# Kernel tuning notes

Hardware: AMD Instinct MI355X
Metric: run time of the kernel (lower is better)

## Reference

```python
import jax, jax.numpy as jnp
import numpy as np

TAU = 1.0
TOP_K = 2

def setup_inputs() -> dict:
    key = jax.random.key(0)
    ks = jax.random.split(key, 5)
    B, C, H, W, E, GH = 16, 64, 128, 128, 8, 16
    return {
        "x": jax.random.normal(ks[0], (B, C, H, W), dtype=jnp.float32),
        "wg1": jax.random.normal(ks[1], (C, GH), dtype=jnp.float32) * 0.1,
        "bg1": jnp.zeros((GH,), dtype=jnp.float32),
        "wg2": jax.random.normal(ks[2], (GH, E), dtype=jnp.float32) * 0.1,
        "bg2": jnp.zeros((E,), dtype=jnp.float32),
        "w_exp": jax.random.normal(ks[3], (E, C, C, 3, 3), dtype=jnp.float32) * 0.05,
        "b_exp": jnp.zeros((E, C), dtype=jnp.float32),
    }

def reference(x, wg1, bg1, wg2, bg2, w_exp, b_exp):
    B, C, H, W = x.shape
    E = w_exp.shape[0]
    # in_proj / out_proj are Identity (c1 == mid_channels == c2)
    x_proj = x
    # gate: GAP -> Linear -> ReLU -> Linear
    pooled = x_proj.mean(axis=(2, 3))                      # [B, C]
    h = jax.nn.relu(pooled @ wg1 + bg1)                    # [B, GH]
    gate_logits = h @ wg2 + bg2                            # [B, E]
    # soft top-k routing (hard=False)
    gate_probs = jax.nn.softmax(gate_logits / TAU, axis=-1)
    _, topk_idx = jax.lax.top_k(gate_probs, TOP_K)         # [B, K]
    mask = jnp.zeros_like(gate_probs).at[jnp.arange(B)[:, None], topk_idx].set(1.0)
    sparse_probs = gate_probs * mask
    sparse_probs = sparse_probs / (sparse_probs.sum(axis=-1, keepdims=True) + 1e-8)
    # dense all-expert 3x3 conv: fold experts into one grouped-output conv
    kern = w_exp.reshape(E * C, C, 3, 3)                   # [E*C, C, 3, 3]
    y = jax.lax.conv_general_dilated(
        x_proj, kern, window_strides=(1, 1), padding="SAME",
        dimension_numbers=("NCHW", "OIHW", "NCHW"))
    y = y.reshape(B, E, C, H, W) + b_exp[None, :, :, None, None]
    # vectorized weighted combine (replaces the per-sample python loop)
    out = jnp.einsum("be,bechw->bchw", sparse_probs, y)
    # shortcut (c1 == c2)
    return out + x
```

## Files before the change

kernel.cpp:

```cpp
#include <hip/hip_runtime.h>
#include <hip/hip_bf16.h>
#include <math.h>

#define B_  16
#define C_  64
#define HW_ 128
#define E_  8
#define GH_ 16

typedef __attribute__((ext_vector_type(8))) short short8;
typedef __attribute__((ext_vector_type(4))) float float4v;

#define ROWS_LDS 4
#define COLS_LDS 132
#define XS_SHORTS (ROWS_LDS * COLS_LDS * 32)
#define WB_PER_B (9 * 2 * 4 * 64 * 8)

__global__ __launch_bounds__(256) void pool_kernel(const float* __restrict__ x,
                                                   float* __restrict__ pooled) {
  const int bc = blockIdx.x;
  const float4v* p4 = (const float4v*)(x + (size_t)bc * (HW_ * HW_));
  float4v s4 = {0.f, 0.f, 0.f, 0.f};
  for (int i = threadIdx.x; i < (HW_ * HW_) / 4; i += 256) s4 += p4[i];
  float s = (s4.x + s4.y) + (s4.z + s4.w);
#pragma unroll
  for (int off = 32; off > 0; off >>= 1) s += __shfl_down(s, off, 64);
  __shared__ float red[4];
  if ((threadIdx.x & 63) == 0) red[threadIdx.x >> 6] = s;
  __syncthreads();
  if (threadIdx.x == 0)
    pooled[bc] = (red[0] + red[1] + red[2] + red[3]) * (1.0f / (HW_ * HW_));
}

__global__ __launch_bounds__(256) void combine_kernel(
    const float* __restrict__ w_exp, const float* __restrict__ pooled,
    const float* __restrict__ wg1, const float* __restrict__ bg1,
    const float* __restrict__ wg2, const float* __restrict__ bg2,
    const float* __restrict__ b_exp, __hip_bfloat16* __restrict__ wB,
    float* __restrict__ bcomb) {
  __shared__ float wtmp[8 * 576];
  __shared__ float hsh[GH_];
  __shared__ float psh[E_];
  const int t = threadIdx.x;
  const int b = blockIdx.x >> 3;
  const int cog = blockIdx.x & 7;

  if (t < GH_) {
    float s = bg1[t];
    for (int c = 0; c < C_; c++)
      s = fmaf(pooled[b * C_ + c], wg1[c * GH_ + t], s);
    hsh[t] = fmaxf(s, 0.f);
  }
  __syncthreads();
  if (t == 0) {
    float p[E_];
    float mx = -1e30f;
#pragma unroll
    for (int e = 0; e < E_; e++) {
      float s = bg2[e];
#pragma unroll
      for (int g = 0; g < GH_; g++) s = fmaf(hsh[g], wg2[g * E_ + e], s);
      p[e] = s;
      mx = fmaxf(mx, s);
    }
    float sum = 0.f;
#pragma unroll
    for (int e = 0; e < E_; e++) { p[e] = expf(p[e] - mx); sum += p[e]; }
    const float inv = 1.0f / sum;
#pragma unroll
    for (int e = 0; e < E_; e++) p[e] *= inv;
    int i1 = 0;
#pragma unroll
    for (int e = 1; e < E_; e++) if (p[e] > p[i1]) i1 = e;
    int i2 = -1;
#pragma unroll
    for (int e = 0; e < E_; e++) {
      if (e == i1) continue;
      if (i2 < 0 || p[e] > p[i2]) i2 = e;
    }
    const float denom = p[i1] + p[i2] + 1e-8f;
#pragma unroll
    for (int e = 0; e < E_; e++)
      psh[e] = (e == i1 || e == i2) ? (p[e] / denom) : 0.f;
  }
  __syncthreads();
  float pb[E_];
#pragma unroll
  for (int e = 0; e < E_; e++) pb[e] = psh[e];

  const size_t src0 = (size_t)cog * 8 * 576;
  for (int i = t; i < 4608; i += 256) {
    float s = 0.f;
#pragma unroll
    for (int e = 0; e < E_; e++)
      s = fmaf(pb[e], w_exp[(size_t)e * (C_ * 576) + src0 + i], s);
    wtmp[i] = s;
  }
  __syncthreads();
  for (int i = t; i < 4608; i += 256) {
    const int j = i & 7;
    const int co_l = (i >> 3) & 7;
    const int rest = i >> 6;
    const int quad = rest & 3;
    const int khalf = (rest >> 2) & 1;
    const int pos = rest >> 3;
    const int ci = khalf * 32 + quad * 8 + j;
    const int co = cog * 8 + co_l;
    float v = wtmp[co_l * 576 + ci * 9 + pos];
    if (pos == 4 && co == ci) v += 1.0f;
    wB[(size_t)b * WB_PER_B +
       ((((pos * 2 + khalf) * 4 + quad) * 64) + co) * 8 + j] =
        __float2bfloat16(v);
  }
  if (t < 8) {
    const int co = cog * 8 + t;
    float s = 0.f;
#pragma unroll
    for (int e = 0; e < E_; e++) s = fmaf(pb[e], b_exp[e * C_ + co], s);
    bcomb[b * C_ + co] = s;
  }
}

__global__ __launch_bounds__(256, 4) void conv_kernel(
    const float* __restrict__ x, const __hip_bfloat16* __restrict__ wB,
    const float* __restrict__ bcomb, float* __restrict__ out) {
  __shared__ __align__(16) short xs[XS_SHORTS];

  const int t = threadIdx.x;
  const int blk = blockIdx.x;
  const int xcd = blk & 7;
  const int idx = blk >> 3;
  const int b = xcd * 2 + (idx >> 6);
  const int strip = idx & 63;
  const int ty = strip * 2;

  const int wave = t >> 6;
  const int L = t & 63;
  const int n16 = L & 15;
  const int quad = L >> 4;

  float bias[4];
#pragma unroll
  for (int nt = 0; nt < 4; nt++) bias[nt] = bcomb[b * C_ + nt * 16 + n16];

  float4v acc[4][4];
#pragma unroll
  for (int mt = 0; mt < 4; mt++)
#pragma unroll
    for (int nt = 0; nt < 4; nt++) acc[mt][nt] = (float4v)0.f;

  for (int h = 0; h < 2; h++) {
    __syncthreads();
#pragma unroll
    for (int it = 0; it < 2; it++) {
      const int i = it * 256 + t;
      const int scq = i & 31;
      const int grp = (i >> 5) & 3;
      const int r = i >> 7;
      const int gh = ty + r - 1;
      const int ci = h * 32 + grp * 8;
      float4v v[8];
      if ((unsigned)gh < (unsigned)HW_) {
        const float* p =
            x + ((size_t)(b * C_ + ci) * HW_ + gh) * HW_ + scq * 4;
#pragma unroll
        for (int k = 0; k < 8; k++)
          v[k] = *(const float4v*)(p + (size_t)k * (HW_ * HW_));
      } else {
#pragma unroll
        for (int k = 0; k < 8; k++) v[k] = (float4v)0.f;
      }
      const int slot = grp ^ (scq & 3);
#pragma unroll
      for (int kk = 0; kk < 4; kk++) {
        const int cl = scq * 4 + kk + 1;
        short8 pk;
#pragma unroll
        for (int k = 0; k < 8; k++) {
          __hip_bfloat16 bb = __float2bfloat16(v[k][kk]);
          pk[k] = *(short*)&bb;
        }
        *(short8*)&xs[((r * COLS_LDS + cl) * 4 + slot) * 8] = pk;
      }
    }
    if (t < 32) {
      const int r = t >> 3;
      const int edge = (t >> 2) & 1;
      const int slot = t & 3;
      const int cl = edge ? 129 : 0;
      *(short8*)&xs[((r * COLS_LDS + cl) * 4 + slot) * 8] = (short8)0;
    }
    __syncthreads();

    const __hip_bfloat16* wBh =
        wB + (size_t)b * WB_PER_B + (size_t)(h * 4 + quad) * 512 + n16 * 8;
    short8 bf[2][4];
#pragma unroll
    for (int nt = 0; nt < 4; nt++)
      bf[0][nt] = *(const short8*)(wBh + nt * 128);

#pragma unroll
    for (int pos = 0; pos < 9; pos++) {
      const int cur = pos & 1;
      if (pos < 8) {
#pragma unroll
        for (int nt = 0; nt < 4; nt++)
          bf[cur ^ 1][nt] =
              *(const short8*)(wBh + (size_t)(pos + 1) * 4096 + nt * 128);
      }
      const int kh = pos / 3;
      const int kw = pos - kh * 3;
      short8 a[4];
#pragma unroll
      for (int mt = 0; mt < 4; mt++) {
        const int mtg = wave * 4 + mt;
        const int lr = (mtg >> 3) + kh;
        const int cl = (mtg & 7) * 16 + n16 + kw;
        const int slot = quad ^ (((cl - 1) >> 2) & 3);
        a[mt] = *(const short8*)&xs[((lr * COLS_LDS + cl) * 4 + slot) * 8];
      }
#pragma unroll
      for (int mt = 0; mt < 4; mt++)
#pragma unroll
        for (int nt = 0; nt < 4; nt++)
          acc[mt][nt] = __builtin_amdgcn_mfma_f32_16x16x32_bf16(
              a[mt], bf[cur][nt], acc[mt][nt], 0, 0, 0);
    }
  }

#pragma unroll
  for (int mtp = 0; mtp < 4; mtp += 2) {
#pragma unroll
    for (int nt = 0; nt < 4; nt++) {
#pragma unroll
      for (int d = 0; d < 2; d++) {
        const int mt = mtp + d;
        const int mtg = wave * 4 + mt;
        const int row = ty + (mtg >> 3);
        const int cb = (mtg & 7) * 16 + quad * 4;
        float4v o = acc[mt][nt];
        o.x += bias[nt];
        o.y += bias[nt];
        o.z += bias[nt];
        o.w += bias[nt];
        *(float4v*)(out +
                    ((size_t)(b * C_ + nt * 16 + n16) * HW_ + row) * HW_ + cb) =
            o;
      }
    }
  }
}

extern "C" void kernel_launch(void* const* d_in, const int* in_sizes, int n_in,
                              void* d_out, int out_size, void* d_ws,
                              size_t ws_size, hipStream_t stream) {
  const float* x     = (const float*)d_in[0];
  const float* wg1   = (const float*)d_in[1];
  const float* bg1   = (const float*)d_in[2];
  const float* wg2   = (const float*)d_in[3];
  const float* bg2   = (const float*)d_in[4];
  const float* w_exp = (const float*)d_in[5];
  const float* b_exp = (const float*)d_in[6];
  float* out = (float*)d_out;

  float* ws = (float*)d_ws;
  float* pooled = ws;
  float* bcomb  = ws + 1024;
  __hip_bfloat16* wB = (__hip_bfloat16*)(ws + 2048);

  pool_kernel<<<B_ * C_, 256, 0, stream>>>(x, pooled);
  combine_kernel<<<B_ * 8, 256, 0, stream>>>(w_exp, pooled, wg1, bg1, wg2, bg2,
                                             b_exp, wB, bcomb);
  conv_kernel<<<1024, 256, 0, stream>>>(x, wB, bcomb, out);
}
```

Before: 188.2 us.

## Split conv tile across 8 waves with fewer M-tiles per wave

The conv block grows from 256 to 512 threads (8 waves). Each wave now owns 2 M-tiles instead of 4, and the LDS staging loop is collapsed so each thread loads one slot. The double-buffered weight prefetch is removed, and the B fragments are loaded per kernel position instead. The aim is to cut register pressure and raise occupancy and latency hiding, at the cost of loading the weight fragments twice as often per block and losing the explicit prefetch overlap.

```diff
diff --git a/kernel.cpp b/kernel.cpp
--- a/kernel.cpp
+++ b/kernel.cpp
@@ -121,7 +121,7 @@
   }
 }
 
-__global__ __launch_bounds__(256, 4) void conv_kernel(
+__global__ __launch_bounds__(512, 8) void conv_kernel(
     const float* __restrict__ x, const __hip_bfloat16* __restrict__ wB,
     const float* __restrict__ bcomb, float* __restrict__ out) {
   __shared__ __align__(16) short xs[XS_SHORTS];
@@ -139,25 +139,24 @@
   const int n16 = L & 15;
   const int quad = L >> 4;
 
+  const int scq = t & 31;
+  const int grp = (t >> 5) & 3;
+  const int sr = t >> 7;
+
   float bias[4];
 #pragma unroll
   for (int nt = 0; nt < 4; nt++) bias[nt] = bcomb[b * C_ + nt * 16 + n16];
 
-  float4v acc[4][4];
-#pragma unroll
-  for (int mt = 0; mt < 4; mt++)
+  float4v acc[2][4];
+#pragma unroll
+  for (int mt = 0; mt < 2; mt++)
 #pragma unroll
     for (int nt = 0; nt < 4; nt++) acc[mt][nt] = (float4v)0.f;
 
   for (int h = 0; h < 2; h++) {
     __syncthreads();
-#pragma unroll
-    for (int it = 0; it < 2; it++) {
-      const int i = it * 256 + t;
-      const int scq = i & 31;
-      const int grp = (i >> 5) & 3;
-      const int r = i >> 7;
-      const int gh = ty + r - 1;
+    {
+      const int gh = ty + sr - 1;
       const int ci = h * 32 + grp * 8;
       float4v v[8];
       if ((unsigned)gh < (unsigned)HW_) {
@@ -180,73 +179,59 @@
           __hip_bfloat16 bb = __float2bfloat16(v[k][kk]);
           pk[k] = *(short*)&bb;
         }
-        *(short8*)&xs[((r * COLS_LDS + cl) * 4 + slot) * 8] = pk;
-      }
-    }
-    if (t < 32) {
-      const int r = t >> 3;
-      const int edge = (t >> 2) & 1;
-      const int slot = t & 3;
-      const int cl = edge ? 129 : 0;
-      *(short8*)&xs[((r * COLS_LDS + cl) * 4 + slot) * 8] = (short8)0;
+        *(short8*)&xs[((sr * COLS_LDS + cl) * 4 + slot) * 8] = pk;
+      }
+      if (t < 32) {
+        const int r = t >> 3;
+        const int edge = (t >> 2) & 1;
+        const int sl = t & 3;
+        const int cl = edge ? 129 : 0;
+        *(short8*)&xs[((r * COLS_LDS + cl) * 4 + sl) * 8] = (short8)0;
+      }
     }
     __syncthreads();
 
     const __hip_bfloat16* wBh =
         wB + (size_t)b * WB_PER_B + (size_t)(h * 4 + quad) * 512 + n16 * 8;
-    short8 bf[2][4];
-#pragma unroll
-    for (int nt = 0; nt < 4; nt++)
-      bf[0][nt] = *(const short8*)(wBh + nt * 128);
 
 #pragma unroll
     for (int pos = 0; pos < 9; pos++) {
-      const int cur = pos & 1;
-      if (pos < 8) {
-#pragma unroll
-        for (int nt = 0; nt < 4; nt++)
-          bf[cur ^ 1][nt] =
-              *(const short8*)(wBh + (size_t)(pos + 1) * 4096 + nt * 128);
-      }
       const int kh = pos / 3;
       const int kw = pos - kh * 3;
-      short8 a[4];
-#pragma unroll
-      for (int mt = 0; mt < 4; mt++) {
-        const int mtg = wave * 4 + mt;
+      short8 bf[4];
+#pragma unroll
+      for (int nt = 0; nt < 4; nt++)
+        bf[nt] = *(const short8*)(wBh + (size_t)pos * 4096 + nt * 128);
+#pragma unroll
+      for (int mt = 0; mt < 2; mt++) {
+        const int mtg = wave * 2 + mt;
         const int lr = (mtg >> 3) + kh;
         const int cl = (mtg & 7) * 16 + n16 + kw;
         const int slot = quad ^ (((cl - 1) >> 2) & 3);
-        a[mt] = *(const short8*)&xs[((lr * COLS_LDS + cl) * 4 + slot) * 8];
-      }
-#pragma unroll
-      for (int mt = 0; mt < 4; mt++)
+        const short8 a =
+            *(const short8*)&xs[((lr * COLS_LDS + cl) * 4 + slot) * 8];
 #pragma unroll
         for (int nt = 0; nt < 4; nt++)
           acc[mt][nt] = __builtin_amdgcn_mfma_f32_16x16x32_bf16(
-              a[mt], bf[cur][nt], acc[mt][nt], 0, 0, 0);
-    }
-  }
-
-#pragma unroll
-  for (int mtp = 0; mtp < 4; mtp += 2) {
+              a, bf[nt], acc[mt][nt], 0, 0, 0);
+      }
+    }
+  }
+
+#pragma unroll
+  for (int mt = 0; mt < 2; mt++) {
+    const int mtg = wave * 2 + mt;
+    const int row = ty + (mtg >> 3);
+    const int cb = (mtg & 7) * 16 + quad * 4;
 #pragma unroll
     for (int nt = 0; nt < 4; nt++) {
-#pragma unroll
-      for (int d = 0; d < 2; d++) {
-        const int mt = mtp + d;
-        const int mtg = wave * 4 + mt;
-        const int row = ty + (mtg >> 3);
-        const int cb = (mtg & 7) * 16 + quad * 4;
-        float4v o = acc[mt][nt];
-        o.x += bias[nt];
-        o.y += bias[nt];
-        o.z += bias[nt];
-        o.w += bias[nt];
-        *(float4v*)(out +
-                    ((size_t)(b * C_ + nt * 16 + n16) * HW_ + row) * HW_ + cb) =
-            o;
-      }
+      float4v o = acc[mt][nt];
+      o.x += bias[nt];
+      o.y += bias[nt];
+      o.z += bias[nt];
+      o.w += bias[nt];
+      *(float4v*)(out +
+                  ((size_t)(b * C_ + nt * 16 + n16) * HW_ + row) * HW_ + cb) = o;
     }
   }
 }
@@ -271,5 +256,5 @@
   pool_kernel<<<B_ * C_, 256, 0, stream>>>(x, pooled);
   combine_kernel<<<B_ * 8, 256, 0, stream>>>(w_exp, pooled, wg1, bg1, wg2, bg2,
                                              b_exp, wB, bcomb);
-  conv_kernel<<<1024, 256, 0, stream>>>(x, wB, bcomb, out);
-}
+  conv_kernel<<<1024, 512, 0, stream>>>(x, wB, bcomb, out);
+}
```

Result: slower. 289.6 us (+53.9%).
